# Optimization experiments

Hardware: AMD Instinct MI355X
Metric: run time of the kernel (lower is better)

Reference implementation:

```python
import jax, jax.numpy as jnp
import numpy as np

E = 2    # non-shared soft experts (nb_soft_experts - nb_shared_experts)
NH = 8   # attention heads
EPS = 1e-6


def _rmsnorm(u, w):
    return u * jax.lax.rsqrt(jnp.mean(u * u, axis=-1, keepdims=True) + EPS) * w


def _rotate(u):
    # torch rotate_embeddings: pairs (x0, x1) -> (-x1, x0), interleaved layout
    p = u.reshape(*u.shape[:-1], -1, 2)[..., ::-1]
    p = p * jnp.array([-1.0, 1.0], dtype=u.dtype)
    return p.reshape(u.shape)


def _rope(u, L, hs):
    # pos = 10000 ** ((-2*arange(0,hs,2) - 1) / hs); rotary = cat(t@pos, t@pos)
    inv = 10000.0 ** ((-2.0 * jnp.arange(0, hs, 2) - 1.0) / hs)      # [hs//2]
    ang = jnp.arange(L)[:, None] * inv[None, :]                      # [L, hs//2]
    rot = jnp.concatenate([ang, ang], axis=-1).astype(u.dtype)       # [L, hs]
    return u * jnp.cos(rot) + _rotate(u) * jnp.sin(rot)


def setup_inputs() -> dict:
    key = jax.random.key(0)
    B, T, C = 2, 2048, 512
    ks = jax.random.split(key, 8)
    s = lambda k_, sh: jax.random.normal(k_, sh, jnp.float32) / np.float32(np.sqrt(sh[0]))
    return dict(
        x=jax.random.normal(ks[0], (B, T, C), jnp.float32),
        W_router=s(ks[1], (C,)),
        W_q=s(ks[2], (C, E * C)),
        W_kv=s(ks[3], (C, 2 * C)),
        W_proj=s(ks[4], (C, C)),
        ln_w=jnp.ones((C,), jnp.float32),
        W_gate=s(ks[5], (C, E)),
        W_pred=s(ks[6], (C,)),
        k=1024,
    )


def reference(x, W_router, W_q, W_kv, W_proj, ln_w, W_gate, W_pred, k):
    B, T, C = x.shape
    hs = C // NH
    # --- MoD router: top-k token selection (apply_top_k_selection) ---
    logits = x @ W_router                                # [B, T]
    vals, idx = jax.lax.top_k(logits, k)                 # [B, k]
    w = jax.nn.sigmoid(vals)
    order = jnp.argsort(idx, axis=1)                     # restore temporal order
    idx = jnp.take_along_axis(idx, order, axis=1)
    w = jnp.take_along_axis(w, order, axis=1)
    sel = jnp.take_along_axis(x, idx[..., None], axis=1)  # gather [B, k, C]
    # --- heavy causal attention branch: E soft-expert queries, shared KV ---
    q = (sel @ W_q).reshape(B, k, E, C).transpose(0, 2, 1, 3)   # [B,E,k,C]
    kk, vv = jnp.split(sel @ W_kv, 2, axis=-1)                  # [B,k,C] each
    q = _rmsnorm(q, ln_w)
    kk = _rmsnorm(kk, ln_w)
    q = q.reshape(B, E, k, NH, hs).transpose(0, 1, 3, 2, 4)     # [B,E,NH,k,hs]
    kk = kk.reshape(B, k, NH, hs).transpose(0, 2, 1, 3)         # [B,NH,k,hs]
    vv = vv.reshape(B, k, NH, hs).transpose(0, 2, 1, 3)
    q = _rope(q, k, hs)
    kk = _rope(kk, k, hs)
    att = jnp.einsum('behqd,bhkd->behqk', q, kk) / np.float32(np.sqrt(hs))
    causal = jnp.tril(jnp.ones((k, k), bool))
    att = jnp.where(causal, att, jnp.finfo(att.dtype).min)
    att = jax.nn.softmax(att, axis=-1)
    y = jnp.einsum('behqk,bhkd->behqd', att, vv)                # [B,E,NH,k,hs]
    y = y.transpose(0, 1, 3, 2, 4).reshape(B, E, k, C) @ W_proj # [B,E,k,C]
    # --- soft-expert combination, router-weight scaling ---
    gate = jax.nn.softmax(sel @ W_gate, axis=-1)                # [B,k,E]
    yc = jnp.einsum('bke,bekc->bkc', gate, y) * w[..., None]    # [B,k,C]
    # --- scatter routed tokens back onto residual stream ---
    out = x.at[jnp.arange(B)[:, None], idx].add(yc)
    # --- sampling predictor BCE loss (calculate_sampling_predictor_loss) ---
    pl = x @ W_pred                                             # [B,T] logits
    tgt = jnp.zeros((B, T), x.dtype).at[jnp.arange(B)[:, None], idx].set(1.0)
    loss = jnp.mean(jnp.maximum(pl, 0) - pl * tgt + jnp.log1p(jnp.exp(-jnp.abs(pl))))
    return out, loss
```

## Files before the change

### kernel.cpp

```cpp
#include <hip/hip_runtime.h>
#include <cstdint>


#define DI __device__ __forceinline__

typedef __bf16 bf16x8 __attribute__((ext_vector_type(8)));
typedef float  f32x4  __attribute__((ext_vector_type(4)));
typedef short  s16x4  __attribute__((ext_vector_type(4)));
typedef short  s16x8  __attribute__((ext_vector_type(8)));

DI uint16_t f2bf(float f) {
    union { float f; uint32_t u; } v; v.f = f;
    uint32_t u = v.u;
    uint32_t r = (u + 0x7FFFu + ((u >> 16) & 1u)) >> 16;
    return (uint16_t)r;
}

DI f32x4 mfma16(bf16x8 a, bf16x8 b, f32x4 c) {
    return __builtin_amdgcn_mfma_f32_16x16x32_bf16(a, b, c, 0, 0, 0);
}
DI f32x4 mfma_k16(s16x4 a, s16x4 b, f32x4 c) {
    return __builtin_amdgcn_mfma_f32_16x16x16bf16_1k(a, b, c, 0, 0, 0);
}
DI void gload16(const void* g, void* l) {
    __builtin_amdgcn_global_load_lds(
        (const __attribute__((address_space(1))) uint32_t*)g,
        (__attribute__((address_space(3))) uint32_t*)l, 16, 0, 0);
}

constexpr size_t OFF_LOGITS = 0;
constexpr size_t OFF_PL     = OFF_LOGITS + 4096 * 4;
constexpr size_t OFF_MASK   = OFF_PL     + 4096 * 4;
constexpr size_t OFF_POSMAP = OFF_MASK   + 4096 * 4;
constexpr size_t OFF_IDX    = OFF_POSMAP + 4096 * 4;
constexpr size_t OFF_WSEL   = OFF_IDX    + 2048 * 4;
constexpr size_t OFF_GATE   = OFF_WSEL   + 2048 * 4;
constexpr size_t OFF_SELBF  = OFF_GATE   + 4096 * 4;
constexpr size_t OFF_WQKVT  = OFF_SELBF  + 2048 * 512 * 2;
constexpr size_t OFF_WPROJT = OFF_WQKVT  + 2048 * 512 * 2;
constexpr size_t OFF_QKVRAW = OFF_WPROJT + 512 * 512 * 2;
constexpr size_t OFF_QH     = OFF_QKVRAW + (size_t)2048 * 2048 * 4;
constexpr size_t OFF_KH     = OFF_QH     + (size_t)2097152 * 2;
constexpr size_t OFF_VT     = OFF_KH     + (size_t)1048576 * 2;
constexpr size_t OFF_YBF    = OFF_VT     + (size_t)1048576 * 2;

__global__ __launch_bounds__(256) void k_prep(const float* __restrict__ Wq,
                                              const float* __restrict__ Wkv,
                                              const float* __restrict__ Wp,
                                              uint16_t* __restrict__ Wqkvt,
                                              uint16_t* __restrict__ Wprojt,
                                              const float4* __restrict__ xsrc,
                                              float4* __restrict__ outdst,
                                              const float* __restrict__ x,
                                              const float* __restrict__ wr,
                                              const float* __restrict__ wp,
                                              float* __restrict__ logits,
                                              float* __restrict__ pl) {
    __shared__ float tile[64][65];
    int blk = blockIdx.x, tid = threadIdx.x;
    if (blk >= 2368) {
        int rblk = blk - 2368;
        int wid  = rblk * 4 + (tid >> 6);
        int lane = tid & 63;
        const float* xr = x + (size_t)wid * 512;
        double s = 0.0; float sp = 0.f;
#pragma unroll
        for (int j = 0; j < 8; j++) {
            int c = lane + 64 * j;
            float xv = xr[c];
            s  += (double)xv * (double)wr[c];
            sp += xv * wp[c];
        }
        for (int m = 1; m < 64; m <<= 1) { s += __shfl_xor(s, m); sp += __shfl_xor(sp, m); }
        if (lane == 0) { logits[wid] = (float)s; pl[wid] = sp; }
        return;
    }
    if (blk >= 320) {
        int j = (blk - 320) * 256 + tid;
        outdst[j] = xsrc[j];
        return;
    }
    const float* src; uint16_t* dst; int n0, c0, ldn;
    if (blk < 256) {
        int tn = blk & 31, tc = blk >> 5;
        n0 = tn * 64; c0 = tc * 64; ldn = 1024;
        if (n0 < 1024) { src = Wq; } else { src = Wkv; n0 -= 1024; }
        dst = Wqkvt + (size_t)(tn * 64) * 512 + c0;
    } else {
        int j = blk - 256; int tn = j & 7, tc = j >> 3;
        n0 = tn * 64; c0 = tc * 64; ldn = 512;
        src = Wp; dst = Wprojt + (size_t)n0 * 512 + c0;
    }
    int nl = tid & 63, cb = tid >> 6;
#pragma unroll
    for (int p = 0; p < 16; p++) {
        int cl_ = p * 4 + cb;
        tile[cl_][nl] = src[(size_t)(c0 + cl_) * ldn + n0 + nl];
    }
    __syncthreads();
    int cp = tid & 31, nb = tid >> 5;
#pragma unroll
    for (int p = 0; p < 8; p++) {
        int nl2 = p * 8 + nb;
        uint32_t pk = (uint32_t)f2bf(tile[cp * 2][nl2]) |
                      ((uint32_t)f2bf(tile[cp * 2 + 1][nl2]) << 16);
        *(uint32_t*)&dst[(size_t)nl2 * 512 + cp * 2] = pk;
    }
}

__global__ void k_rank(const float* __restrict__ logits, int* __restrict__ mask) {
    int wid  = (blockIdx.x * blockDim.x + threadIdx.x) >> 6;
    int lane = threadIdx.x & 63;
    if (wid >= 4096) return;
    int b = wid >> 11, t = wid & 2047;
    const float* lb = logits + b * 2048;
    float v = lb[t];
    int cnt = 0;
    for (int j = 0; j < 32; j++) {
        int tp = lane + 64 * j;
        float lv = lb[tp];
        bool pred = (lv > v) || (lv == v && tp < t);
        cnt += __popcll(__ballot(pred));
    }
    if (lane == 0) mask[wid] = (cnt < 1024) ? 1 : 0;
}

__global__ void k_select(const float* __restrict__ logits, const int* __restrict__ mask,
                         int* __restrict__ idx, float* __restrict__ wsel,
                         int* __restrict__ posmap) {
    __shared__ int wsum[16], woff[16];
    int b = blockIdx.x, tid = threadIdx.x, lane = tid & 63, w = tid >> 6;
    int t0 = tid * 2, t1 = tid * 2 + 1;
    int m0 = mask[b * 2048 + t0], m1 = mask[b * 2048 + t1];
    int s = m0 + m1;
    int sc = s;
    for (int off = 1; off < 64; off <<= 1) {
        int v = __shfl_up(sc, off);
        if (lane >= off) sc += v;
    }
    if (lane == 63) wsum[w] = sc;
    __syncthreads();
    if (tid < 16) {
        int acc = 0;
        for (int j = 0; j < tid; j++) acc += wsum[j];
        woff[tid] = acc;
    }
    __syncthreads();
    int excl = woff[w] + sc - s;
    int p0 = excl, p1 = excl + m0;
    if (m0) {
        idx[b * 1024 + p0] = t0;
        float v = logits[b * 2048 + t0];
        wsel[b * 1024 + p0] = 1.f / (1.f + __expf(-v));
    }
    posmap[b * 2048 + t0] = m0 ? p0 : -1;
    if (m1) {
        idx[b * 1024 + p1] = t1;
        float v = logits[b * 2048 + t1];
        wsel[b * 1024 + p1] = 1.f / (1.f + __expf(-v));
    }
    posmap[b * 2048 + t1] = m1 ? p1 : -1;
}

__global__ void k_gather_gate(const float* __restrict__ x, const int* __restrict__ idx,
                              const float* __restrict__ Wg,
                              uint16_t* __restrict__ selbf, float* __restrict__ gate) {
    __shared__ float red0[4], red1[4];
    int blk = blockIdx.x; int b = blk >> 10;
    int tid = threadIdx.x, lane = tid & 63, w = tid >> 6;
    int t = idx[blk];
    const float* xr = x + ((size_t)b * 2048 + t) * 512;
    int c = tid * 2;
    float v0 = xr[c], v1 = xr[c + 1];
    uint32_t pk = (uint32_t)f2bf(v0) | ((uint32_t)f2bf(v1) << 16);
    ((uint32_t*)(selbf + (size_t)blk * 512))[tid] = pk;
    float g0 = v0 * Wg[c * 2]     + v1 * Wg[(c + 1) * 2];
    float g1 = v0 * Wg[c * 2 + 1] + v1 * Wg[(c + 1) * 2 + 1];
    for (int m = 1; m < 64; m <<= 1) { g0 += __shfl_xor(g0, m); g1 += __shfl_xor(g1, m); }
    if (lane == 0) { red0[w] = g0; red1[w] = g1; }
    __syncthreads();
    if (tid == 0) {
        float a = red0[0] + red0[1] + red0[2] + red0[3];
        float bq = red1[0] + red1[1] + red1[2] + red1[3];
        float mx = fmaxf(a, bq);
        float ea = __expf(a - mx), eb = __expf(bq - mx), s = ea + eb;
        gate[blk * 2] = ea / s; gate[blk * 2 + 1] = eb / s;
    }
}

__global__ __launch_bounds__(256) void k_gemm(const uint16_t* __restrict__ A,
                                              const uint16_t* __restrict__ Bt,
                                              float* __restrict__ Cc,
                                              int M, int N, int Kd) {
    __shared__ uint16_t As[128 * 32];
    __shared__ uint16_t Bs[64 * 32];
    int tid = threadIdx.x, lane = tid & 63, w = tid >> 6;
    int m0 = blockIdx.x * 128, n0 = blockIdx.y * 64;
    int wr = (w >> 1) * 64, wc = (w & 1) * 32;
    int cl = lane & 15, gp = lane >> 4;
    f32x4 acc[4][2];
#pragma unroll
    for (int mt = 0; mt < 4; mt++)
#pragma unroll
        for (int nt = 0; nt < 2; nt++)
#pragma unroll
            for (int r = 0; r < 4; r++) acc[mt][nt][r] = 0.f;
    int srow = lane >> 2, skc = (lane & 3) * 8;
    for (int ks = 0; ks < Kd; ks += 32) {
        __syncthreads();
        const uint16_t* ga0 = A + (size_t)(m0 + w * 32 + srow) * Kd + ks + skc;
        gload16(ga0, &As[(w * 32) * 32]);
        gload16(ga0 + (size_t)16 * Kd, &As[(w * 32 + 16) * 32]);
        const uint16_t* gb = Bt + (size_t)(n0 + w * 16 + srow) * Kd + ks + skc;
        gload16(gb, &Bs[(w * 16) * 32]);
        __syncthreads();
        bf16x8 af[4], bfr[2];
#pragma unroll
        for (int t = 0; t < 4; t++)
            af[t] = *(const bf16x8*)&As[(wr + t * 16 + cl) * 32 + gp * 8];
#pragma unroll
        for (int t = 0; t < 2; t++)
            bfr[t] = *(const bf16x8*)&Bs[(wc + t * 16 + cl) * 32 + gp * 8];
#pragma unroll
        for (int mt = 0; mt < 4; mt++)
#pragma unroll
            for (int nt = 0; nt < 2; nt++)
                acc[mt][nt] = mfma16(af[mt], bfr[nt], acc[mt][nt]);
    }
    int r0 = gp * 4;
#pragma unroll
    for (int mt = 0; mt < 4; mt++)
#pragma unroll
        for (int nt = 0; nt < 2; nt++)
#pragma unroll
            for (int r = 0; r < 4; r++) {
                int row = m0 + wr + mt * 16 + r0 + r;
                int col = n0 + wc + nt * 16 + cl;
                Cc[(size_t)row * N + col] = acc[mt][nt][r];
            }
}

__global__ __launch_bounds__(256) void k_nrv(const float* __restrict__ qkv,
                                             const float* __restrict__ lnw,
                                             uint16_t* __restrict__ Qh,
                                             uint16_t* __restrict__ Kh,
                                             uint16_t* __restrict__ Vt) {
    __shared__ float tile[64][65];
    int blk = blockIdx.x, tid = threadIdx.x;
    if (blk >= 2048) {
        int v = blk - 2048;
        int bh = v >> 4, kt = v & 15;
        int b = bh >> 3, h = bh & 7;
        int r = tid >> 2, cg = tid & 3;
        const float* srow = qkv + ((size_t)(b * 1024 + kt * 64 + r)) * 2048 + 1536 + h * 64 + cg * 16;
#pragma unroll
        for (int p = 0; p < 4; p++) {
            float4 vv = *(const float4*)(srow + p * 4);
            tile[r][cg * 16 + p * 4 + 0] = vv.x;
            tile[r][cg * 16 + p * 4 + 1] = vv.y;
            tile[r][cg * 16 + p * 4 + 2] = vv.z;
            tile[r][cg * 16 + p * 4 + 3] = vv.w;
        }
        __syncthreads();
        int d = tid >> 2, t4 = tid & 3;
        uint16_t* drow = Vt + ((size_t)(bh * 64 + d)) * 1024 + kt * 64;
#pragma unroll
        for (int g = 0; g < 4; g++) {
            uint16_t pk[4];
#pragma unroll
            for (int j = 0; j < 4; j++) pk[j] = f2bf(tile[t4 * 16 + g * 4 + j][d]);
            *(uint2*)&drow[g * 16 + t4 * 4] = *(const uint2*)pk;
        }
        return;
    }
    int b = blk >> 10, i = blk & 1023;
    int lane = tid & 63, w = tid >> 6;
    float* red = &tile[0][0];
    const float* row = qkv + (size_t)blk * 2048;
    int c0 = tid * 2;
    int d0 = c0 & 63, head = c0 >> 6;
    int j0 = d0 & 31, j1 = (d0 + 1) & 31;
    const float LN1E4_64 = 0.14391156831212787f;
    float fi = (float)i;
    float ang0 = fi * __expf(-(float)(4 * j0 + 1) * LN1E4_64);
    float ang1 = fi * __expf(-(float)(4 * j1 + 1) * LN1E4_64);
    float c_0 = cosf(ang0), s_0 = sinf(ang0);
    float c_1 = cosf(ang1), s_1 = sinf(ang1);
    float g0 = lnw[c0], g1 = lnw[c0 + 1];
    for (int which = 0; which < 3; which++) {
        int off = which * 512;
        float u0 = row[off + c0], u1 = row[off + c0 + 1];
        float ss = u0 * u0 + u1 * u1;
        for (int m = 1; m < 64; m <<= 1) ss += __shfl_xor(ss, m);
        __syncthreads();
        if (lane == 0) red[w] = ss;
        __syncthreads();
        float tot = red[0] + red[1] + red[2] + red[3];
        float rinv = rsqrtf(tot * (1.0f / 512.0f) + 1e-6f);
        float n0 = u0 * rinv * g0, n1 = u1 * rinv * g1;
        float r0 = n0 * c_0 - n1 * s_0;
        float r1 = n1 * c_1 + n0 * s_1;
        if (which < 2) {
            uint32_t pk = (uint32_t)f2bf(r0) | ((uint32_t)f2bf(r1) << 16);
            uint16_t* dstp = Qh + ((size_t)((b * 2 + which) * 8 + head) * 1024 + i) * 64 + d0;
            *(uint32_t*)dstp = pk;
        } else {
            uint32_t pk = (uint32_t)f2bf(r0 * 0.125f) | ((uint32_t)f2bf(r1 * 0.125f) << 16);
            uint16_t* dstp = Kh + ((size_t)(b * 8 + head) * 1024 + i) * 64 + d0;
            *(uint32_t*)dstp = pk;
        }
    }
}

__global__ __launch_bounds__(512, 4) void k_attn(const uint16_t* __restrict__ Qh,
                                                 const uint16_t* __restrict__ Kh,
                                                 const uint16_t* __restrict__ Vt,
                                                 uint16_t* __restrict__ ybf) {
    __shared__ float cb[3][2][64][17];
    int blk = blockIdx.x;
    int pj = blk >> 5;
    int inst = blk & 31;
    int h = inst & 7, b = inst >> 4;
    int tid = threadIdx.x, lane = tid & 63, w = tid >> 6;
    int wq = w & 1, ws = w >> 1;
    const uint16_t* Kb = Kh + (size_t)(b * 8 + h) * 1024 * 64;
    const uint16_t* Vb = Vt + (size_t)(b * 8 + h) * 64 * 1024;
    int cl = lane & 15, gp = lane >> 4;
    const float L2E = 1.44269504f;
    const float SH  = -11.5415603f;

#pragma unroll
    for (int ph = 0; ph < 2; ph++) {
        int qt = ph ? pj : (31 - pj);
        int qw = qt * 32 + wq * 16;
        const uint16_t* Qb = Qh + ((size_t)inst * 1024 + qw) * 64;
        bf16x8 qf0 = *(const bf16x8*)&Qb[cl * 64 + gp * 8];
        bf16x8 qf1 = *(const bf16x8*)&Qb[cl * 64 + 32 + gp * 8];
        f32x4 o[4];
#pragma unroll
        for (int dt = 0; dt < 4; dt++)
#pragma unroll
            for (int r = 0; r < 4; r++) o[dt][r] = 0.f;
        float ls = 0.f;
        int qa = qw + cl;

        for (int jt = ws * 64; jt <= qw; jt += 256) {
            bf16x8 kf[8];
            s16x8 vv0[4], vv1[4];
#pragma unroll
            for (int t = 0; t < 4; t++) {
                const uint16_t* kr = &Kb[(size_t)(jt + t * 16 + cl) * 64 + gp * 8];
                kf[t * 2]     = *(const bf16x8*)kr;
                kf[t * 2 + 1] = *(const bf16x8*)(kr + 32);
            }
#pragma unroll
            for (int dt = 0; dt < 4; dt++) {
                const uint16_t* vrow = &Vb[(size_t)(dt * 16 + cl) * 1024 + jt + gp * 16];
                vv0[dt] = *(const s16x8*)vrow;
                vv1[dt] = *(const s16x8*)(vrow + 8);
            }
            f32x4 sv[4];
#pragma unroll
            for (int t = 0; t < 4; t++)
#pragma unroll
                for (int r = 0; r < 4; r++) sv[t][r] = 0.f;
#pragma unroll
            for (int t = 0; t < 4; t++) {
                sv[t] = mfma16(kf[t * 2], qf0, sv[t]);
                sv[t] = mfma16(kf[t * 2 + 1], qf1, sv[t]);
            }
            bool bnd = (jt + 63 > qw);
            s16x4 pb[4];
#pragma unroll
            for (int t = 0; t < 4; t++) {
                union { s16x4 s4; __bf16 bf[4]; } pu;
#pragma unroll
                for (int r = 0; r < 4; r++) {
                    float p = exp2f(fmaf(sv[t][r], L2E, SH));
                    if (bnd) {
                        int kv = jt + t * 16 + gp * 4 + r;
                        p = (kv <= qa) ? p : 0.f;
                    }
                    ls += p;
                    pu.bf[r] = (__bf16)p;
                }
                pb[t] = pu.s4;
            }
#pragma unroll
            for (int dt = 0; dt < 4; dt++) {
                s16x4 a0 = __builtin_shufflevector(vv0[dt], vv0[dt], 0, 1, 2, 3);
                s16x4 a1 = __builtin_shufflevector(vv0[dt], vv0[dt], 4, 5, 6, 7);
                s16x4 a2 = __builtin_shufflevector(vv1[dt], vv1[dt], 0, 1, 2, 3);
                s16x4 a3 = __builtin_shufflevector(vv1[dt], vv1[dt], 4, 5, 6, 7);
                o[dt] = mfma_k16(a0, pb[0], o[dt]);
                o[dt] = mfma_k16(a1, pb[1], o[dt]);
                o[dt] = mfma_k16(a2, pb[2], o[dt]);
                o[dt] = mfma_k16(a3, pb[3], o[dt]);
            }
        }
        ls += __shfl_xor(ls, 16);
        ls += __shfl_xor(ls, 32);
        if (ws != 0) {
#pragma unroll
            for (int dt = 0; dt < 4; dt++)
#pragma unroll
                for (int r = 0; r < 4; r++) cb[ws - 1][wq][lane][dt * 4 + r] = o[dt][r];
            cb[ws - 1][wq][lane][16] = ls;
        }
        __syncthreads();
        if (ws == 0) {
            float lst = ls + cb[0][wq][lane][16] + cb[1][wq][lane][16] + cb[2][wq][lane][16];
            float inv = 1.f / lst;
            uint16_t* yb = ybf + ((size_t)((inst >> 3) * 1024 + qw)) * 512 + h * 64;
#pragma unroll
            for (int dt = 0; dt < 4; dt++) {
                uint16_t pk[4];
#pragma unroll
                for (int r = 0; r < 4; r++) {
                    float v = o[dt][r] + cb[0][wq][lane][dt * 4 + r]
                                       + cb[1][wq][lane][dt * 4 + r]
                                       + cb[2][wq][lane][dt * 4 + r];
                    pk[r] = f2bf(v * inv);
                }
                *(uint2*)&yb[(size_t)cl * 512 + dt * 16 + gp * 4] = *(const uint2*)pk;
            }
        }
        __syncthreads();
    }
}

__global__ __launch_bounds__(256) void k_projc(const uint16_t* __restrict__ ybf,
                                               const uint16_t* __restrict__ Wprojt,
                                               const int* __restrict__ idx,
                                               const float* __restrict__ wsel,
                                               const float* __restrict__ gate,
                                               const float* __restrict__ x,
                                               const float* __restrict__ pl,
                                               const int* __restrict__ mask,
                                               float* __restrict__ out) {
    __shared__ uint16_t As0[64 * 40], As1[64 * 40], Bs[64 * 40];
    int pid = blockIdx.x;
    int tid = threadIdx.x;
    if (pid == 32) {
        if (blockIdx.y != 0) return;
        __shared__ float red[4];
        int lane = tid & 63, wl = tid >> 6;
        float s = 0.f;
#pragma unroll
        for (int j = 0; j < 16; j++) {
            int i = tid * 16 + j;
            float p = pl[i];
            float tgt = (float)mask[i];
            s += fmaxf(p, 0.f) - p * tgt + log1pf(__expf(-fabsf(p)));
        }
        for (int mm = 1; mm < 64; mm <<= 1) s += __shfl_xor(s, mm);
        if (lane == 0) red[wl] = s;
        __syncthreads();
        if (tid == 0)
            out[2097152] = (red[0] + red[1] + red[2] + red[3]) * (1.0f / 4096.0f);
        return;
    }
    int b = pid >> 4, pos0 = (pid & 15) * 64;
    int n0 = blockIdx.y * 64;
    int lane = tid & 63, w = tid >> 6;
    int cl = lane & 15, gp = lane >> 4;
    f32x4 acc0[4], acc1[4];
#pragma unroll
    for (int nt = 0; nt < 4; nt++)
#pragma unroll
        for (int r = 0; r < 4; r++) { acc0[nt][r] = 0.f; acc1[nt][r] = 0.f; }
    int arow = tid >> 2, akg = tid & 3;
    const bf16x8* A8 = (const bf16x8*)ybf;
    const bf16x8* B8 = (const bf16x8*)Wprojt;
    size_t rowe0 = (size_t)(b * 2) * 1024 + pos0 + arow;
    for (int ks = 0; ks < 512; ks += 32) {
        __syncthreads();
        int kc = (ks >> 3) + akg;
        bf16x8 va0 = A8[rowe0 * 64 + kc];
        bf16x8 va1 = A8[(rowe0 + 1024) * 64 + kc];
        bf16x8 vb  = B8[(size_t)(n0 + arow) * 64 + kc];
        *(bf16x8*)&As0[arow * 40 + akg * 8] = va0;
        *(bf16x8*)&As1[arow * 40 + akg * 8] = va1;
        *(bf16x8*)&Bs[arow * 40 + akg * 8]  = vb;
        __syncthreads();
        bf16x8 a0 = *(const bf16x8*)&As0[(w * 16 + cl) * 40 + gp * 8];
        bf16x8 a1 = *(const bf16x8*)&As1[(w * 16 + cl) * 40 + gp * 8];
#pragma unroll
        for (int nt = 0; nt < 4; nt++) {
            bf16x8 bfr = *(const bf16x8*)&Bs[(nt * 16 + cl) * 40 + gp * 8];
            acc0[nt] = mfma16(a0, bfr, acc0[nt]);
            acc1[nt] = mfma16(a1, bfr, acc1[nt]);
        }
    }
#pragma unroll
    for (int r = 0; r < 4; r++) {
        int pos = pos0 + w * 16 + gp * 4 + r;
        int bk = b * 1024 + pos;
        int t = idx[bk];
        float wv = wsel[bk], g0 = gate[bk * 2], g1 = gate[bk * 2 + 1];
        const float* xrow = x + ((size_t)(b * 2048 + t)) * 512;
        float* orow = out + ((size_t)(b * 2048 + t)) * 512;
#pragma unroll
        for (int nt = 0; nt < 4; nt++) {
            int col = n0 + nt * 16 + cl;
            orow[col] = xrow[col] + wv * (g0 * acc0[nt][r] + g1 * acc1[nt][r]);
        }
    }
}

extern "C" void kernel_launch(void* const* d_in, const int* in_sizes, int n_in,
                              void* d_out, int out_size, void* d_ws, size_t ws_size,
                              hipStream_t stream) {
    const float* x        = (const float*)d_in[0];
    const float* W_router = (const float*)d_in[1];
    const float* W_q      = (const float*)d_in[2];
    const float* W_kv     = (const float*)d_in[3];
    const float* W_proj   = (const float*)d_in[4];
    const float* ln_w     = (const float*)d_in[5];
    const float* W_gate   = (const float*)d_in[6];
    const float* W_pred   = (const float*)d_in[7];

    char* ws = (char*)d_ws;
    float*    logits = (float*)   (ws + OFF_LOGITS);
    float*    pl     = (float*)   (ws + OFF_PL);
    int*      mask   = (int*)     (ws + OFF_MASK);
    int*      posmap = (int*)     (ws + OFF_POSMAP);
    int*      idx    = (int*)     (ws + OFF_IDX);
    float*    wsel   = (float*)   (ws + OFF_WSEL);
    float*    gate   = (float*)   (ws + OFF_GATE);
    uint16_t* selbf  = (uint16_t*)(ws + OFF_SELBF);
    uint16_t* Wqkvt  = (uint16_t*)(ws + OFF_WQKVT);
    uint16_t* Wprojt = (uint16_t*)(ws + OFF_WPROJT);
    float*    qkvraw = (float*)   (ws + OFF_QKVRAW);
    uint16_t* Qh     = (uint16_t*)(ws + OFF_QH);
    uint16_t* Kh     = (uint16_t*)(ws + OFF_KH);
    uint16_t* Vt     = (uint16_t*)(ws + OFF_VT);
    uint16_t* ybf    = (uint16_t*)(ws + OFF_YBF);
    float*    out    = (float*)d_out;

    k_prep       <<<3392, 256, 0, stream>>>(W_q, W_kv, W_proj, Wqkvt, Wprojt,
                                            (const float4*)x, (float4*)out,
                                            x, W_router, W_pred, logits, pl);
    k_rank       <<<1024, 256, 0, stream>>>(logits, mask);
    k_select     <<<2, 1024, 0, stream>>>(logits, mask, idx, wsel, posmap);
    k_gather_gate<<<2048, 256, 0, stream>>>(x, idx, W_gate, selbf, gate);
    k_gemm       <<<dim3(16, 32), 256, 0, stream>>>(selbf, Wqkvt, qkvraw, 2048, 2048, 512);
    k_nrv        <<<2304, 256, 0, stream>>>(qkvraw, ln_w, Qh, Kh, Vt);
    k_attn       <<<512, 512, 0, stream>>>(Qh, Kh, Vt, ybf);
    k_projc      <<<dim3(33, 8), 256, 0, stream>>>(ybf, Wprojt, idx, wsel, gate, x,
                                                   pl, mask, out);
}
```

Baseline: 94.42 us.

## Share K/V tiles across both experts in attention; copy only unselected residual rows

The attention kernel now gives each block one query tile and both expert queries. The K/V fragments it loads are reused for two score/PV passes, instead of loading them separately per expert while pairing a long and a short query tile per block. This roughly halves K/V global traffic but doubles accumulator registers (launch bound lowered to 2 waves-per-SIMD occupancy target) and drops the causal load-balancing pairing. Separately, the x-to-out residual copy moves from the prep kernel into the gather kernel and only copies rows not selected by the router, since selected rows are written by the projection kernel.

```diff
diff --git a/kernel.cpp b/kernel.cpp
--- a/kernel.cpp
+++ b/kernel.cpp
@@ -49,8 +49,6 @@
                                               const float* __restrict__ Wp,
                                               uint16_t* __restrict__ Wqkvt,
                                               uint16_t* __restrict__ Wprojt,
-                                              const float4* __restrict__ xsrc,
-                                              float4* __restrict__ outdst,
                                               const float* __restrict__ x,
                                               const float* __restrict__ wr,
                                               const float* __restrict__ wp,
@@ -58,8 +56,8 @@
                                               float* __restrict__ pl) {
     __shared__ float tile[64][65];
     int blk = blockIdx.x, tid = threadIdx.x;
-    if (blk >= 2368) {
-        int rblk = blk - 2368;
+    if (blk >= 320) {
+        int rblk = blk - 320;
         int wid  = rblk * 4 + (tid >> 6);
         int lane = tid & 63;
         const float* xr = x + (size_t)wid * 512;
@@ -73,11 +71,6 @@
         }
         for (int m = 1; m < 64; m <<= 1) { s += __shfl_xor(s, m); sp += __shfl_xor(sp, m); }
         if (lane == 0) { logits[wid] = (float)s; pl[wid] = sp; }
-        return;
-    }
-    if (blk >= 320) {
-        int j = (blk - 320) * 256 + tid;
-        outdst[j] = xsrc[j];
         return;
     }
     const float* src; uint16_t* dst; int n0, c0, ldn;
@@ -163,11 +156,23 @@
 }
 
 __global__ void k_gather_gate(const float* __restrict__ x, const int* __restrict__ idx,
-                              const float* __restrict__ Wg,
-                              uint16_t* __restrict__ selbf, float* __restrict__ gate) {
+                              const float* __restrict__ Wg, const int* __restrict__ posmap,
+                              uint16_t* __restrict__ selbf, float* __restrict__ gate,
+                              float* __restrict__ out) {
     __shared__ float red0[4], red1[4];
-    int blk = blockIdx.x; int b = blk >> 10;
+    int blk = blockIdx.x;
     int tid = threadIdx.x, lane = tid & 63, w = tid >> 6;
+    if (blk >= 2048) {
+        int row = (blk - 2048) * 2 + (tid >> 7);
+        int ci = tid & 127;
+        if (posmap[row] < 0) {
+            const float4* xr = (const float4*)(x + (size_t)row * 512);
+            float4* orow = (float4*)(out + (size_t)row * 512);
+            orow[ci] = xr[ci];
+        }
+        return;
+    }
+    int b = blk >> 10;
     int t = idx[blk];
     const float* xr = x + ((size_t)b * 2048 + t) * 512;
     int c = tid * 2;
@@ -312,64 +317,68 @@
     }
 }
 
-__global__ __launch_bounds__(512, 4) void k_attn(const uint16_t* __restrict__ Qh,
+__global__ __launch_bounds__(512, 2) void k_attn(const uint16_t* __restrict__ Qh,
                                                  const uint16_t* __restrict__ Kh,
                                                  const uint16_t* __restrict__ Vt,
                                                  uint16_t* __restrict__ ybf) {
-    __shared__ float cb[3][2][64][17];
+    __shared__ float cb[2][3][2][64][17];
     int blk = blockIdx.x;
-    int pj = blk >> 5;
-    int inst = blk & 31;
-    int h = inst & 7, b = inst >> 4;
+    int qt = 31 - (blk >> 4);
+    int inst = blk & 15;
+    int h = inst & 7, b = inst >> 3;
     int tid = threadIdx.x, lane = tid & 63, w = tid >> 6;
     int wq = w & 1, ws = w >> 1;
-    const uint16_t* Kb = Kh + (size_t)(b * 8 + h) * 1024 * 64;
-    const uint16_t* Vb = Vt + (size_t)(b * 8 + h) * 64 * 1024;
+    int qw = qt * 32 + wq * 16;
+    const uint16_t* Kb = Kh + (size_t)inst * 1024 * 64;
+    const uint16_t* Vb = Vt + (size_t)inst * 64 * 1024;
     int cl = lane & 15, gp = lane >> 4;
+    const uint16_t* Qb0 = Qh + ((size_t)((b * 2 + 0) * 8 + h) * 1024 + qw) * 64;
+    const uint16_t* Qb1 = Qh + ((size_t)((b * 2 + 1) * 8 + h) * 1024 + qw) * 64;
+    bf16x8 qf00 = *(const bf16x8*)&Qb0[cl * 64 + gp * 8];
+    bf16x8 qf01 = *(const bf16x8*)&Qb0[cl * 64 + 32 + gp * 8];
+    bf16x8 qf10 = *(const bf16x8*)&Qb1[cl * 64 + gp * 8];
+    bf16x8 qf11 = *(const bf16x8*)&Qb1[cl * 64 + 32 + gp * 8];
+    f32x4 o0[4], o1[4];
+#pragma unroll
+    for (int dt = 0; dt < 4; dt++)
+#pragma unroll
+        for (int r = 0; r < 4; r++) { o0[dt][r] = 0.f; o1[dt][r] = 0.f; }
+    float ls0 = 0.f, ls1 = 0.f;
+    int qa = qw + cl;
     const float L2E = 1.44269504f;
     const float SH  = -11.5415603f;
 
-#pragma unroll
-    for (int ph = 0; ph < 2; ph++) {
-        int qt = ph ? pj : (31 - pj);
-        int qw = qt * 32 + wq * 16;
-        const uint16_t* Qb = Qh + ((size_t)inst * 1024 + qw) * 64;
-        bf16x8 qf0 = *(const bf16x8*)&Qb[cl * 64 + gp * 8];
-        bf16x8 qf1 = *(const bf16x8*)&Qb[cl * 64 + 32 + gp * 8];
-        f32x4 o[4];
-#pragma unroll
-        for (int dt = 0; dt < 4; dt++)
-#pragma unroll
-            for (int r = 0; r < 4; r++) o[dt][r] = 0.f;
-        float ls = 0.f;
-        int qa = qw + cl;
-
-        for (int jt = ws * 64; jt <= qw; jt += 256) {
-            bf16x8 kf[8];
-            s16x8 vv0[4], vv1[4];
-#pragma unroll
-            for (int t = 0; t < 4; t++) {
-                const uint16_t* kr = &Kb[(size_t)(jt + t * 16 + cl) * 64 + gp * 8];
-                kf[t * 2]     = *(const bf16x8*)kr;
-                kf[t * 2 + 1] = *(const bf16x8*)(kr + 32);
-            }
-#pragma unroll
-            for (int dt = 0; dt < 4; dt++) {
-                const uint16_t* vrow = &Vb[(size_t)(dt * 16 + cl) * 1024 + jt + gp * 16];
-                vv0[dt] = *(const s16x8*)vrow;
-                vv1[dt] = *(const s16x8*)(vrow + 8);
-            }
+    for (int jt = ws * 64; jt <= qw; jt += 256) {
+        s16x8 vv0[4], vv1[4];
+        const uint16_t* kr0 = &Kb[(size_t)(jt + cl) * 64 + gp * 8];
+        const uint16_t* kr1 = &Kb[(size_t)(jt + 16 + cl) * 64 + gp * 8];
+        const uint16_t* kr2 = &Kb[(size_t)(jt + 32 + cl) * 64 + gp * 8];
+        const uint16_t* kr3 = &Kb[(size_t)(jt + 48 + cl) * 64 + gp * 8];
+        bf16x8 k00 = *(const bf16x8*)kr0, k01 = *(const bf16x8*)(kr0 + 32);
+        bf16x8 k10 = *(const bf16x8*)kr1, k11 = *(const bf16x8*)(kr1 + 32);
+        bf16x8 k20 = *(const bf16x8*)kr2, k21 = *(const bf16x8*)(kr2 + 32);
+        bf16x8 k30 = *(const bf16x8*)kr3, k31 = *(const bf16x8*)(kr3 + 32);
+#pragma unroll
+        for (int dt = 0; dt < 4; dt++) {
+            const uint16_t* vrow = &Vb[(size_t)(dt * 16 + cl) * 1024 + jt + gp * 16];
+            vv0[dt] = *(const s16x8*)vrow;
+            vv1[dt] = *(const s16x8*)(vrow + 8);
+        }
+        bool bnd = (jt + 63 > qw);
+#pragma unroll
+        for (int e = 0; e < 2; e++) {
+            bf16x8 qa0 = e ? qf10 : qf00;
+            bf16x8 qa1 = e ? qf11 : qf01;
             f32x4 sv[4];
 #pragma unroll
             for (int t = 0; t < 4; t++)
 #pragma unroll
                 for (int r = 0; r < 4; r++) sv[t][r] = 0.f;
-#pragma unroll
-            for (int t = 0; t < 4; t++) {
-                sv[t] = mfma16(kf[t * 2], qf0, sv[t]);
-                sv[t] = mfma16(kf[t * 2 + 1], qf1, sv[t]);
-            }
-            bool bnd = (jt + 63 > qw);
+            sv[0] = mfma16(k00, qa0, sv[0]); sv[0] = mfma16(k01, qa1, sv[0]);
+            sv[1] = mfma16(k10, qa0, sv[1]); sv[1] = mfma16(k11, qa1, sv[1]);
+            sv[2] = mfma16(k20, qa0, sv[2]); sv[2] = mfma16(k21, qa1, sv[2]);
+            sv[3] = mfma16(k30, qa0, sv[3]); sv[3] = mfma16(k31, qa1, sv[3]);
+            float lsl = 0.f;
             s16x4 pb[4];
 #pragma unroll
             for (int t = 0; t < 4; t++) {
@@ -381,51 +390,63 @@
                         int kv = jt + t * 16 + gp * 4 + r;
                         p = (kv <= qa) ? p : 0.f;
                     }
-                    ls += p;
+                    lsl += p;
                     pu.bf[r] = (__bf16)p;
                 }
                 pb[t] = pu.s4;
             }
+            if (e == 0) ls0 += lsl; else ls1 += lsl;
 #pragma unroll
             for (int dt = 0; dt < 4; dt++) {
                 s16x4 a0 = __builtin_shufflevector(vv0[dt], vv0[dt], 0, 1, 2, 3);
                 s16x4 a1 = __builtin_shufflevector(vv0[dt], vv0[dt], 4, 5, 6, 7);
                 s16x4 a2 = __builtin_shufflevector(vv1[dt], vv1[dt], 0, 1, 2, 3);
                 s16x4 a3 = __builtin_shufflevector(vv1[dt], vv1[dt], 4, 5, 6, 7);
-                o[dt] = mfma_k16(a0, pb[0], o[dt]);
-                o[dt] = mfma_k16(a1, pb[1], o[dt]);
-                o[dt] = mfma_k16(a2, pb[2], o[dt]);
-                o[dt] = mfma_k16(a3, pb[3], o[dt]);
+                f32x4 oo = e ? o1[dt] : o0[dt];
+                oo = mfma_k16(a0, pb[0], oo);
+                oo = mfma_k16(a1, pb[1], oo);
+                oo = mfma_k16(a2, pb[2], oo);
+                oo = mfma_k16(a3, pb[3], oo);
+                if (e == 0) o0[dt] = oo; else o1[dt] = oo;
             }
         }
-        ls += __shfl_xor(ls, 16);
-        ls += __shfl_xor(ls, 32);
-        if (ws != 0) {
-#pragma unroll
-            for (int dt = 0; dt < 4; dt++)
-#pragma unroll
-                for (int r = 0; r < 4; r++) cb[ws - 1][wq][lane][dt * 4 + r] = o[dt][r];
-            cb[ws - 1][wq][lane][16] = ls;
-        }
-        __syncthreads();
-        if (ws == 0) {
-            float lst = ls + cb[0][wq][lane][16] + cb[1][wq][lane][16] + cb[2][wq][lane][16];
+    }
+    ls0 += __shfl_xor(ls0, 16); ls0 += __shfl_xor(ls0, 32);
+    ls1 += __shfl_xor(ls1, 16); ls1 += __shfl_xor(ls1, 32);
+    if (ws != 0) {
+#pragma unroll
+        for (int dt = 0; dt < 4; dt++)
+#pragma unroll
+            for (int r = 0; r < 4; r++) {
+                cb[0][ws - 1][wq][lane][dt * 4 + r] = o0[dt][r];
+                cb[1][ws - 1][wq][lane][dt * 4 + r] = o1[dt][r];
+            }
+        cb[0][ws - 1][wq][lane][16] = ls0;
+        cb[1][ws - 1][wq][lane][16] = ls1;
+    }
+    __syncthreads();
+    if (ws == 0) {
+#pragma unroll
+        for (int e = 0; e < 2; e++) {
+            float lse = e ? ls1 : ls0;
+            float lst = lse + cb[e][0][wq][lane][16] + cb[e][1][wq][lane][16]
+                            + cb[e][2][wq][lane][16];
             float inv = 1.f / lst;
-            uint16_t* yb = ybf + ((size_t)((inst >> 3) * 1024 + qw)) * 512 + h * 64;
+            uint16_t* yb = ybf + ((size_t)((b * 2 + e) * 1024 + qw)) * 512 + h * 64;
 #pragma unroll
             for (int dt = 0; dt < 4; dt++) {
                 uint16_t pk[4];
 #pragma unroll
                 for (int r = 0; r < 4; r++) {
-                    float v = o[dt][r] + cb[0][wq][lane][dt * 4 + r]
-                                       + cb[1][wq][lane][dt * 4 + r]
-                                       + cb[2][wq][lane][dt * 4 + r];
+                    float base = e ? o1[dt][r] : o0[dt][r];
+                    float v = base + cb[e][0][wq][lane][dt * 4 + r]
+                                   + cb[e][1][wq][lane][dt * 4 + r]
+                                   + cb[e][2][wq][lane][dt * 4 + r];
                     pk[r] = f2bf(v * inv);
                 }
                 *(uint2*)&yb[(size_t)cl * 512 + dt * 16 + gp * 4] = *(const uint2*)pk;
             }
         }
-        __syncthreads();
     }
 }
 
@@ -538,12 +559,11 @@
     uint16_t* ybf    = (uint16_t*)(ws + OFF_YBF);
     float*    out    = (float*)d_out;
 
-    k_prep       <<<3392, 256, 0, stream>>>(W_q, W_kv, W_proj, Wqkvt, Wprojt,
-                                            (const float4*)x, (float4*)out,
+    k_prep       <<<1344, 256, 0, stream>>>(W_q, W_kv, W_proj, Wqkvt, Wprojt,
                                             x, W_router, W_pred, logits, pl);
     k_rank       <<<1024, 256, 0, stream>>>(logits, mask);
     k_select     <<<2, 1024, 0, stream>>>(logits, mask, idx, wsel, posmap);
-    k_gather_gate<<<2048, 256, 0, stream>>>(x, idx, W_gate, selbf, gate);
+    k_gather_gate<<<4096, 256, 0, stream>>>(x, idx, W_gate, posmap, selbf, gate, out);
     k_gemm       <<<dim3(16, 32), 256, 0, stream>>>(selbf, Wqkvt, qkvraw, 2048, 2048, 512);
     k_nrv        <<<2304, 256, 0, stream>>>(qkvraw, ln_w, Qh, Kh, Vt);
     k_attn       <<<512, 512, 0, stream>>>(Qh, Kh, Vt, ybf);
```

After: 82.59 us (median of 2 runs). 12.5% less time.

## Share K/V across experts in attention blocks and copy only unselected residual rows

Applied to the files above, without the earlier changes.

The attention kernel is rewritten so each block handles one query tile for both soft experts of a (batch, head) pair. Warps are split across expert, query half and a two-way KV split, so each K/V tile is loaded once for both experts, replacing the paired-tile, four-way KV-split scheme. The full x-to-out copy in the prep kernel is replaced by a copy inside the gather kernel that writes only rows not selected by the router, which cuts memory traffic. Trade-offs: blocks no longer pair short and long causal tiles, which risks load imbalance. Correctness also assumes the projection kernel writes x plus the update for selected rows.

```diff
diff --git a/kernel.cpp b/kernel.cpp
--- a/kernel.cpp
+++ b/kernel.cpp
@@ -49,8 +49,6 @@
                                               const float* __restrict__ Wp,
                                               uint16_t* __restrict__ Wqkvt,
                                               uint16_t* __restrict__ Wprojt,
-                                              const float4* __restrict__ xsrc,
-                                              float4* __restrict__ outdst,
                                               const float* __restrict__ x,
                                               const float* __restrict__ wr,
                                               const float* __restrict__ wp,
@@ -58,8 +56,8 @@
                                               float* __restrict__ pl) {
     __shared__ float tile[64][65];
     int blk = blockIdx.x, tid = threadIdx.x;
-    if (blk >= 2368) {
-        int rblk = blk - 2368;
+    if (blk >= 320) {
+        int rblk = blk - 320;
         int wid  = rblk * 4 + (tid >> 6);
         int lane = tid & 63;
         const float* xr = x + (size_t)wid * 512;
@@ -73,11 +71,6 @@
         }
         for (int m = 1; m < 64; m <<= 1) { s += __shfl_xor(s, m); sp += __shfl_xor(sp, m); }
         if (lane == 0) { logits[wid] = (float)s; pl[wid] = sp; }
-        return;
-    }
-    if (blk >= 320) {
-        int j = (blk - 320) * 256 + tid;
-        outdst[j] = xsrc[j];
         return;
     }
     const float* src; uint16_t* dst; int n0, c0, ldn;
@@ -163,11 +156,23 @@
 }
 
 __global__ void k_gather_gate(const float* __restrict__ x, const int* __restrict__ idx,
-                              const float* __restrict__ Wg,
-                              uint16_t* __restrict__ selbf, float* __restrict__ gate) {
+                              const float* __restrict__ Wg, const int* __restrict__ posmap,
+                              uint16_t* __restrict__ selbf, float* __restrict__ gate,
+                              float* __restrict__ out) {
     __shared__ float red0[4], red1[4];
-    int blk = blockIdx.x; int b = blk >> 10;
+    int blk = blockIdx.x;
     int tid = threadIdx.x, lane = tid & 63, w = tid >> 6;
+    if (blk >= 2048) {
+        int row = (blk - 2048) * 2 + (tid >> 7);
+        int ci = tid & 127;
+        if (posmap[row] < 0) {
+            const float4* xr = (const float4*)(x + (size_t)row * 512);
+            float4* orow = (float4*)(out + (size_t)row * 512);
+            orow[ci] = xr[ci];
+        }
+        return;
+    }
+    int b = blk >> 10;
     int t = idx[blk];
     const float* xr = x + ((size_t)b * 2048 + t) * 512;
     int c = tid * 2;
@@ -312,120 +317,108 @@
     }
 }
 
-__global__ __launch_bounds__(512, 4) void k_attn(const uint16_t* __restrict__ Qh,
+__global__ __launch_bounds__(512, 2) void k_attn(const uint16_t* __restrict__ Qh,
                                                  const uint16_t* __restrict__ Kh,
                                                  const uint16_t* __restrict__ Vt,
                                                  uint16_t* __restrict__ ybf) {
-    __shared__ float cb[3][2][64][17];
+    __shared__ float cb[2][2][64][17];
     int blk = blockIdx.x;
-    int pj = blk >> 5;
-    int inst = blk & 31;
-    int h = inst & 7, b = inst >> 4;
+    int qt = 31 - (blk >> 4);
+    int inst = blk & 15;
+    int h = inst & 7, b = inst >> 3;
     int tid = threadIdx.x, lane = tid & 63, w = tid >> 6;
-    int wq = w & 1, ws = w >> 1;
-    const uint16_t* Kb = Kh + (size_t)(b * 8 + h) * 1024 * 64;
-    const uint16_t* Vb = Vt + (size_t)(b * 8 + h) * 64 * 1024;
+    int wq = w & 1, e = (w >> 1) & 1, ws = w >> 2;
+    int qw = qt * 32 + wq * 16;
+    const uint16_t* Kb = Kh + (size_t)inst * 1024 * 64;
+    const uint16_t* Vb = Vt + (size_t)inst * 64 * 1024;
     int cl = lane & 15, gp = lane >> 4;
+    const uint16_t* Qb = Qh + ((size_t)((b * 2 + e) * 8 + h) * 1024 + qw) * 64;
+    bf16x8 qf0 = *(const bf16x8*)&Qb[cl * 64 + gp * 8];
+    bf16x8 qf1 = *(const bf16x8*)&Qb[cl * 64 + 32 + gp * 8];
+    f32x4 o[4];
+#pragma unroll
+    for (int dt = 0; dt < 4; dt++)
+#pragma unroll
+        for (int r = 0; r < 4; r++) o[dt][r] = 0.f;
+    float ls = 0.f;
+    int qa = qw + cl;
     const float L2E = 1.44269504f;
     const float SH  = -11.5415603f;
 
-#pragma unroll
-    for (int ph = 0; ph < 2; ph++) {
-        int qt = ph ? pj : (31 - pj);
-        int qw = qt * 32 + wq * 16;
-        const uint16_t* Qb = Qh + ((size_t)inst * 1024 + qw) * 64;
-        bf16x8 qf0 = *(const bf16x8*)&Qb[cl * 64 + gp * 8];
-        bf16x8 qf1 = *(const bf16x8*)&Qb[cl * 64 + 32 + gp * 8];
-        f32x4 o[4];
+    for (int jt = ws * 64; jt <= qw; jt += 128) {
+        s16x8 vv0[4], vv1[4];
+#pragma unroll
+        for (int dt = 0; dt < 4; dt++) {
+            const uint16_t* vrow = &Vb[(size_t)(dt * 16 + cl) * 1024 + jt + gp * 16];
+            vv0[dt] = *(const s16x8*)vrow;
+            vv1[dt] = *(const s16x8*)(vrow + 8);
+        }
+        f32x4 sv[4];
+#pragma unroll
+        for (int t = 0; t < 4; t++)
+#pragma unroll
+            for (int r = 0; r < 4; r++) sv[t][r] = 0.f;
+#pragma unroll
+        for (int t = 0; t < 4; t++) {
+            const uint16_t* kr = &Kb[(size_t)(jt + t * 16 + cl) * 64 + gp * 8];
+            bf16x8 k0 = *(const bf16x8*)kr;
+            bf16x8 k1 = *(const bf16x8*)(kr + 32);
+            sv[t] = mfma16(k0, qf0, sv[t]);
+            sv[t] = mfma16(k1, qf1, sv[t]);
+        }
+        bool bnd = (jt + 63 > qw);
+        s16x4 pb[4];
+#pragma unroll
+        for (int t = 0; t < 4; t++) {
+            union { s16x4 s4; __bf16 bf[4]; } pu;
+#pragma unroll
+            for (int r = 0; r < 4; r++) {
+                float p = exp2f(fmaf(sv[t][r], L2E, SH));
+                if (bnd) {
+                    int kv = jt + t * 16 + gp * 4 + r;
+                    p = (kv <= qa) ? p : 0.f;
+                }
+                ls += p;
+                pu.bf[r] = (__bf16)p;
+            }
+            pb[t] = pu.s4;
+        }
+#pragma unroll
+        for (int dt = 0; dt < 4; dt++) {
+            s16x4 a0 = __builtin_shufflevector(vv0[dt], vv0[dt], 0, 1, 2, 3);
+            s16x4 a1 = __builtin_shufflevector(vv0[dt], vv0[dt], 4, 5, 6, 7);
+            s16x4 a2 = __builtin_shufflevector(vv1[dt], vv1[dt], 0, 1, 2, 3);
+            s16x4 a3 = __builtin_shufflevector(vv1[dt], vv1[dt], 4, 5, 6, 7);
+            o[dt] = mfma_k16(a0, pb[0], o[dt]);
+            o[dt] = mfma_k16(a1, pb[1], o[dt]);
+            o[dt] = mfma_k16(a2, pb[2], o[dt]);
+            o[dt] = mfma_k16(a3, pb[3], o[dt]);
+        }
+    }
+    ls += __shfl_xor(ls, 16);
+    ls += __shfl_xor(ls, 32);
+    if (ws == 1) {
 #pragma unroll
         for (int dt = 0; dt < 4; dt++)
 #pragma unroll
-            for (int r = 0; r < 4; r++) o[dt][r] = 0.f;
-        float ls = 0.f;
-        int qa = qw + cl;
-
-        for (int jt = ws * 64; jt <= qw; jt += 256) {
-            bf16x8 kf[8];
-            s16x8 vv0[4], vv1[4];
-#pragma unroll
-            for (int t = 0; t < 4; t++) {
-                const uint16_t* kr = &Kb[(size_t)(jt + t * 16 + cl) * 64 + gp * 8];
-                kf[t * 2]     = *(const bf16x8*)kr;
-                kf[t * 2 + 1] = *(const bf16x8*)(kr + 32);
+            for (int r = 0; r < 4; r++) cb[e][wq][lane][dt * 4 + r] = o[dt][r];
+        cb[e][wq][lane][16] = ls;
+    }
+    __syncthreads();
+    if (ws == 0) {
+        float lst = ls + cb[e][wq][lane][16];
+        float inv = 1.f / lst;
+        uint16_t* yb = ybf + ((size_t)((b * 2 + e) * 1024 + qw)) * 512 + h * 64;
+#pragma unroll
+        for (int dt = 0; dt < 4; dt++) {
+            uint16_t pk[4];
+#pragma unroll
+            for (int r = 0; r < 4; r++) {
+                float v = o[dt][r] + cb[e][wq][lane][dt * 4 + r];
+                pk[r] = f2bf(v * inv);
             }
-#pragma unroll
-            for (int dt = 0; dt < 4; dt++) {
-                const uint16_t* vrow = &Vb[(size_t)(dt * 16 + cl) * 1024 + jt + gp * 16];
-                vv0[dt] = *(const s16x8*)vrow;
-                vv1[dt] = *(const s16x8*)(vrow + 8);
-            }
-            f32x4 sv[4];
-#pragma unroll
-            for (int t = 0; t < 4; t++)
-#pragma unroll
-                for (int r = 0; r < 4; r++) sv[t][r] = 0.f;
-#pragma unroll
-            for (int t = 0; t < 4; t++) {
-                sv[t] = mfma16(kf[t * 2], qf0, sv[t]);
-                sv[t] = mfma16(kf[t * 2 + 1], qf1, sv[t]);
-            }
-            bool bnd = (jt + 63 > qw);
-            s16x4 pb[4];
-#pragma unroll
-            for (int t = 0; t < 4; t++) {
-                union { s16x4 s4; __bf16 bf[4]; } pu;
-#pragma unroll
-                for (int r = 0; r < 4; r++) {
-                    float p = exp2f(fmaf(sv[t][r], L2E, SH));
-                    if (bnd) {
-                        int kv = jt + t * 16 + gp * 4 + r;
-                        p = (kv <= qa) ? p : 0.f;
-                    }
-                    ls += p;
-                    pu.bf[r] = (__bf16)p;
-                }
-                pb[t] = pu.s4;
-            }
-#pragma unroll
-            for (int dt = 0; dt < 4; dt++) {
-                s16x4 a0 = __builtin_shufflevector(vv0[dt], vv0[dt], 0, 1, 2, 3);
-                s16x4 a1 = __builtin_shufflevector(vv0[dt], vv0[dt], 4, 5, 6, 7);
-                s16x4 a2 = __builtin_shufflevector(vv1[dt], vv1[dt], 0, 1, 2, 3);
-                s16x4 a3 = __builtin_shufflevector(vv1[dt], vv1[dt], 4, 5, 6, 7);
-                o[dt] = mfma_k16(a0, pb[0], o[dt]);
-                o[dt] = mfma_k16(a1, pb[1], o[dt]);
-                o[dt] = mfma_k16(a2, pb[2], o[dt]);
-                o[dt] = mfma_k16(a3, pb[3], o[dt]);
-            }
-        }
-        ls += __shfl_xor(ls, 16);
-        ls += __shfl_xor(ls, 32);
-        if (ws != 0) {
-#pragma unroll
-            for (int dt = 0; dt < 4; dt++)
-#pragma unroll
-                for (int r = 0; r < 4; r++) cb[ws - 1][wq][lane][dt * 4 + r] = o[dt][r];
-            cb[ws - 1][wq][lane][16] = ls;
-        }
-        __syncthreads();
-        if (ws == 0) {
-            float lst = ls + cb[0][wq][lane][16] + cb[1][wq][lane][16] + cb[2][wq][lane][16];
-            float inv = 1.f / lst;
-            uint16_t* yb = ybf + ((size_t)((inst >> 3) * 1024 + qw)) * 512 + h * 64;
-#pragma unroll
-            for (int dt = 0; dt < 4; dt++) {
-                uint16_t pk[4];
-#pragma unroll
-                for (int r = 0; r < 4; r++) {
-                    float v = o[dt][r] + cb[0][wq][lane][dt * 4 + r]
-                                       + cb[1][wq][lane][dt * 4 + r]
-                                       + cb[2][wq][lane][dt * 4 + r];
-                    pk[r] = f2bf(v * inv);
-                }
-                *(uint2*)&yb[(size_t)cl * 512 + dt * 16 + gp * 4] = *(const uint2*)pk;
-            }
-        }
-        __syncthreads();
+            *(uint2*)&yb[(size_t)cl * 512 + dt * 16 + gp * 4] = *(const uint2*)pk;
+        }
     }
 }
 
@@ -538,12 +531,11 @@
     uint16_t* ybf    = (uint16_t*)(ws + OFF_YBF);
     float*    out    = (float*)d_out;
 
-    k_prep       <<<3392, 256, 0, stream>>>(W_q, W_kv, W_proj, Wqkvt, Wprojt,
-                                            (const float4*)x, (float4*)out,
+    k_prep       <<<1344, 256, 0, stream>>>(W_q, W_kv, W_proj, Wqkvt, Wprojt,
                                             x, W_router, W_pred, logits, pl);
     k_rank       <<<1024, 256, 0, stream>>>(logits, mask);
     k_select     <<<2, 1024, 0, stream>>>(logits, mask, idx, wsel, posmap);
-    k_gather_gate<<<2048, 256, 0, stream>>>(x, idx, W_gate, selbf, gate);
+    k_gather_gate<<<4096, 256, 0, stream>>>(x, idx, W_gate, posmap, selbf, gate, out);
     k_gemm       <<<dim3(16, 32), 256, 0, stream>>>(selbf, Wqkvt, qkvraw, 2048, 2048, 512);
     k_nrv        <<<2304, 256, 0, stream>>>(qkvraw, ln_w, Qh, Kh, Vt);
     k_attn       <<<512, 512, 0, stream>>>(Qh, Kh, Vt, ybf);
```

Result: slower. 104.5 us (+10.7%).
